# Performance work log

Measured on AMD Instinct MI355X. Metric: run time of the kernel, lower is better.

## Reference

```python
import jax, jax.numpy as jnp
import numpy as np

HEADS = 16
DIM_HEAD = 64
SCALE = DIM_HEAD ** -0.5
TEMPERATURE = 1.0
CAUSAL = True


def setup_inputs() -> dict:
    key = jax.random.key(0)
    k_x, k_qkv, k_out, k_len = jax.random.split(key, 4)
    B, N, D = 2, 2048, 1024
    inner = HEADS * DIM_HEAD  # 1024
    x = jax.random.normal(k_x, (B, N, D), dtype=jnp.float32)
    # realistic key-padding mask: True for valid tokens (variable lengths)
    lengths = jax.random.randint(k_len, (B,), N // 2, N + 1)
    mask = jnp.arange(N)[None, :] < lengths[:, None]  # (B, N) bool
    W_qkv = jax.random.normal(k_qkv, (D, 3 * inner), dtype=jnp.float32) * (D ** -0.5)
    W_out = jax.random.normal(k_out, (inner, D), dtype=jnp.float32) * (inner ** -0.5)
    b_out = jnp.zeros((D,), dtype=jnp.float32)
    return {"x": x, "mask": mask, "W_qkv": W_qkv, "W_out": W_out, "b_out": b_out}


def reference(x, mask, W_qkv, W_out, b_out):
    B, N, D = x.shape
    qkv = x @ W_qkv  # (B, N, 3*inner)
    q, k, v = jnp.split(qkv, 3, axis=-1)
    # (B, N, H*d) -> (B, H, N, d)
    def split_heads(t):
        return t.reshape(B, N, HEADS, DIM_HEAD).transpose(0, 2, 1, 3)
    q, k, v = split_heads(q), split_heads(k), split_heads(v)
    q = q * SCALE
    dots = jnp.einsum('bhid,bhjd->bhij', q, k)  # (B, H, N, N)
    mask_value = -jnp.finfo(dots.dtype).max
    # key padding mask: True = valid; mask invalid keys
    dots = jnp.where(mask[:, None, None, :], dots, mask_value)
    if CAUSAL:
        causal = jnp.arange(N)[None, :] > jnp.arange(N)[:, None]  # True = future -> masked
        dots = jnp.where(causal[None, None, :, :], mask_value, dots)
    # stable softmax with temperature (jax.nn.softmax subtracts max internally)
    attn = jax.nn.softmax(dots / TEMPERATURE, axis=-1)
    out = jnp.einsum('bhij,bhjd->bhid', attn, v)  # (B, H, N, d)
    out = out.transpose(0, 2, 1, 3).reshape(B, N, HEADS * DIM_HEAD)
    return out @ W_out + b_out
```

## Files before the change

kernel.cpp:

```cpp
#include <hip/hip_runtime.h>

#define BATCH   2
#define NSEQ    2048
#define DMODEL  1024
#define HEADS   16
#define DHEAD   64
#define INNER   1024
#define NCOL    3072
#define BNROWS  4096
#define KDIM    1024

typedef unsigned short ushort;
typedef unsigned int   uint;
typedef __attribute__((ext_vector_type(8)))  short  short8;
typedef __attribute__((ext_vector_type(4)))  float  f32x4;
typedef __attribute__((ext_vector_type(16))) float  f32x16;
typedef __attribute__((ext_vector_type(8)))  ushort ushort8;
typedef __attribute__((ext_vector_type(4)))  float  f4v;
typedef __attribute__((ext_vector_type(4)))  uint   uint4v;

#define QSCALE 0.1803368801111204f

__device__ __forceinline__ ushort f2bf(float f) {
  uint u = __builtin_bit_cast(uint, f);
  u += 0x7fffu + ((u >> 16) & 1u);
  return (ushort)(u >> 16);
}
__device__ __forceinline__ uint cvtpk(float a, float b) {
  uint r;
  asm("v_cvt_pk_bf16_f32 %0, %1, %2" : "=v"(r) : "v"(a), "v"(b));
  return r;
}

__device__ __forceinline__ f32x4 mfma16(short8 a, short8 b, f32x4 c) {
  return __builtin_amdgcn_mfma_f32_16x16x32_bf16(a, b, c, 0, 0, 0);
}
__device__ __forceinline__ f32x16 mfma32(short8 a, short8 b, f32x16 c) {
  return __builtin_amdgcn_mfma_f32_32x32x16_bf16(a, b, c, 0, 0, 0);
}

#define GLDS(gp, lp) __builtin_amdgcn_global_load_lds( \
    (const __attribute__((address_space(1))) void*)(gp), \
    (__attribute__((address_space(3))) void*)(lp), 16, 0, 0)

__global__ __launch_bounds__(256) void lens_kernel(const int* __restrict__ mask,
                                                   int* __restrict__ lens) {
  __shared__ int sm[256];
  int b = blockIdx.x, t = threadIdx.x;
  int s = 0;
  for (int i = t; i < NSEQ; i += 256) s += (mask[b * NSEQ + i] != 0);
  sm[t] = s;
  __syncthreads();
  for (int off = 128; off > 0; off >>= 1) {
    if (t < off) sm[t] += sm[t + off];
    __syncthreads();
  }
  if (t == 0) lens[b] = sm[0];
}

__global__ __launch_bounds__(256) void cast_bf16_kernel(const float* __restrict__ x,
                                                        ushort* __restrict__ y, int n8) {
  int i = blockIdx.x * 256 + threadIdx.x;
  if (i >= n8) return;
  const f4v* xv = (const f4v*)x;
  f4v a = xv[(size_t)i * 2], b = xv[(size_t)i * 2 + 1];
  ushort8 o;
  o[0] = f2bf(a[0]); o[1] = f2bf(a[1]); o[2] = f2bf(a[2]); o[3] = f2bf(a[3]);
  o[4] = f2bf(b[0]); o[5] = f2bf(b[1]); o[6] = f2bf(b[2]); o[7] = f2bf(b[3]);
  ((ushort8*)y)[i] = o;
}

__global__ __launch_bounds__(256) void transpose_bf16_kernel(const float* __restrict__ W,
                                                             ushort* __restrict__ Wt,
                                                             int K, int C) {
  __shared__ float tile[32][33];
  int c0 = blockIdx.x * 32, k0 = blockIdx.y * 32;
  int tx = threadIdx.x, ty = threadIdx.y;
#pragma unroll
  for (int i = 0; i < 4; ++i)
    tile[ty + i * 8][tx] = W[(size_t)(k0 + ty + i * 8) * C + c0 + tx];
  __syncthreads();
#pragma unroll
  for (int i = 0; i < 4; ++i)
    Wt[(size_t)(c0 + ty + i * 8) * K + k0 + tx] = f2bf(tile[tx][ty + i * 8]);
}

__global__ __launch_bounds__(256) void vtrans_kernel(const ushort* __restrict__ v,
                                                     ushort* __restrict__ vt) {
  __shared__ ushort t[32][34];
  int d0 = blockIdx.x * 32, n0 = blockIdx.y * 32, bh = blockIdx.z;
  const ushort* vb  = v  + (size_t)bh * NSEQ * DHEAD;
  ushort*       vtb = vt + (size_t)bh * NSEQ * DHEAD;
  int tx = threadIdx.x, ty = threadIdx.y;
#pragma unroll
  for (int i = 0; i < 4; ++i)
    t[ty + i * 8][tx] = vb[(size_t)(n0 + ty + i * 8) * DHEAD + d0 + tx];
  __syncthreads();
#pragma unroll
  for (int i = 0; i < 4; ++i)
    vtb[(size_t)(d0 + ty + i * 8) * NSEQ + n0 + tx] = t[tx][ty + i * 8];
}

template <int EPI>
__global__ __launch_bounds__(256) void gemm_bt_kernel(
    const ushort* __restrict__ A, const ushort* __restrict__ Bt,
    ushort* __restrict__ q_out, ushort* __restrict__ k_out, ushort* __restrict__ v_out,
    const float* __restrict__ bias, float* __restrict__ outp) {
  __shared__ __align__(16) ushort lA[128 * 64];
  __shared__ __align__(16) ushort lB[128 * 64];
  const int tid = threadIdx.x;
  const int wv = tid >> 6, lane = tid & 63;
  const int wr = wv >> 1, wc = wv & 1;
  const int m0 = blockIdx.x * 128, n0 = blockIdx.y * 128;
  const int l15 = lane & 15, l4 = lane >> 4;

  f32x4 zero = {0.f, 0.f, 0.f, 0.f};
  f32x4 acc[4][4];
#pragma unroll
  for (int i = 0; i < 4; ++i)
#pragma unroll
    for (int j = 0; j < 4; ++j) acc[i][j] = zero;

  const char* Ab  = (const char*)A;
  const char* Bb  = (const char*)Bt;
  char* lAb = (char*)lA;
  char* lBb = (char*)lB;

  for (int kt = 0; kt < KDIM; kt += 64) {
#pragma unroll
    for (int t = 0; t < 4; ++t) {
      int o = wv * 4096 + t * 1024 + lane * 16;
      int row = o >> 7, cb = o & 127;
      GLDS(Ab + ((size_t)(m0 + row) * KDIM + kt) * 2 + cb, lAb + o);
      GLDS(Bb + ((size_t)(n0 + row) * KDIM + kt) * 2 + cb, lBb + o);
    }
    __syncthreads();

    short8 af[4][2], bfr[4][2];
#pragma unroll
    for (int i = 0; i < 4; ++i) {
#pragma unroll
      for (int kc = 0; kc < 2; ++kc) {
        af[i][kc]  = *(const short8*)(lAb + (wr * 64 + i * 16 + l15) * 128 + kc * 64 + l4 * 16);
        bfr[i][kc] = *(const short8*)(lBb + (wc * 64 + i * 16 + l15) * 128 + kc * 64 + l4 * 16);
      }
    }
#pragma unroll
    for (int i = 0; i < 4; ++i)
#pragma unroll
      for (int j = 0; j < 4; ++j)
#pragma unroll
        for (int kc = 0; kc < 2; ++kc)
          acc[i][j] = mfma16(af[i][kc], bfr[j][kc], acc[i][j]);
    __syncthreads();
  }

#pragma unroll
  for (int i = 0; i < 4; ++i) {
#pragma unroll
    for (int j = 0; j < 4; ++j) {
#pragma unroll
      for (int r = 0; r < 4; ++r) {
        int grow = m0 + wr * 64 + i * 16 + l4 * 4 + r;
        int gcol = n0 + wc * 64 + j * 16 + l15;
        float v = acc[i][j][r];
        if (EPI == 0) {
          int b = grow >> 11, n = grow & (NSEQ - 1);
          int which = gcol >> 10, inner = gcol & 1023;
          int h = inner >> 6, dd = inner & 63;
          size_t off = ((size_t)(b * HEADS + h) * NSEQ + n) * DHEAD + dd;
          if (which == 0)
            q_out[off] = f2bf(v * QSCALE);
          else if (which == 1)
            k_out[off] = f2bf(v);
          else
            v_out[off] = f2bf(v);
        } else {
          outp[(size_t)grow * INNER + gcol] = v + bias[gcol];
        }
      }
    }
  }
}

__global__ __launch_bounds__(64) void attn_kernel(
    const ushort* __restrict__ q, const ushort* __restrict__ k,
    const ushort* __restrict__ vt, const int* __restrict__ lens,
    ushort* __restrict__ ctx) {
  const int lane = threadIdx.x;
  const int l31 = lane & 31, hi = lane >> 5;
  const int bid = blockIdx.x;
  const int bh = bid & 31, qt = bid >> 5;
  const int b = bh >> 4, h = bh & 15;
  const int len = lens[b];
  const ushort* qb  = q  + (size_t)bh * NSEQ * DHEAD;
  const ushort* kbp = k  + (size_t)bh * NSEQ * DHEAD;
  const ushort* vtb = vt + (size_t)bh * DHEAD * NSEQ;

  const int qglob = qt * 32 + l31;
  const int qcap  = min(qglob, len - 1);

  short8 qf[4];
#pragma unroll
  for (int dk = 0; dk < 4; ++dk)
    qf[dk] = *(const short8*)&qb[(size_t)(qt * 32 + l31) * DHEAD + dk * 16 + hi * 8];

  f32x16 Ot[2];
#pragma unroll
  for (int d0b = 0; d0b < 2; ++d0b)
#pragma unroll
    for (int r = 0; r < 16; ++r) Ot[d0b][r] = 0.f;
  float mrow = -3.0e38f, lsum = 0.f;

  const int kbend = min(qt, (len - 1) >> 5);

  short8 kf[4], kn[4];
#pragma unroll
  for (int dk = 0; dk < 4; ++dk)
    kf[dk] = *(const short8*)&kbp[(size_t)l31 * DHEAD + dk * 16 + hi * 8];

  for (int kb = 0; kb <= kbend; ++kb) {
    f32x16 S;
#pragma unroll
    for (int r = 0; r < 16; ++r) S[r] = 0.f;
#pragma unroll
    for (int dk = 0; dk < 4; ++dk) S = mfma32(kf[dk], qf[dk], S);

    short8 vf[2][2];
#pragma unroll
    for (int d0b = 0; d0b < 2; ++d0b)
#pragma unroll
      for (int ks = 0; ks < 2; ++ks)
        vf[d0b][ks] = *(const short8*)&vtb[(size_t)(d0b * 32 + l31) * NSEQ +
                                           kb * 32 + ks * 16 + hi * 8];

    {
      int kread = min(kb + 1, kbend);
#pragma unroll
      for (int dk = 0; dk < 4; ++dk)
        kn[dk] = *(const short8*)&kbp[(size_t)(kread * 32 + l31) * DHEAD + dk * 16 + hi * 8];
    }

    bool fast = (kb < qt) && (kb * 32 + 31 < len);
    if (!fast) {
      int base = kb * 32 + 4 * hi;
#pragma unroll
      for (int r = 0; r < 16; ++r) {
        int c = (r & 3) + 8 * (r >> 2);
        if (base + c > qcap) S[r] = -3.0e38f;
      }
    }

    float t0 = fmaxf(S[0], S[1]),  t1 = fmaxf(S[2], S[3]);
    float t2 = fmaxf(S[4], S[5]),  t3 = fmaxf(S[6], S[7]);
    float t4 = fmaxf(S[8], S[9]),  t5 = fmaxf(S[10], S[11]);
    float t6 = fmaxf(S[12], S[13]), t7 = fmaxf(S[14], S[15]);
    t0 = fmaxf(t0, t1); t2 = fmaxf(t2, t3); t4 = fmaxf(t4, t5); t6 = fmaxf(t6, t7);
    float pm = fmaxf(fmaxf(t0, t2), fmaxf(t4, t6));
    pm = fmaxf(pm, __shfl_xor(pm, 32));

    if (!__all(pm <= mrow + 8.0f)) {
      float mnew = fmaxf(mrow, pm);
      float scale = exp2f(mrow - mnew);
      lsum *= scale;
#pragma unroll
      for (int d0b = 0; d0b < 2; ++d0b)
#pragma unroll
        for (int r = 0; r < 16; ++r) Ot[d0b][r] *= scale;
      mrow = mnew;
    }

    float p[16];
#pragma unroll
    for (int r = 0; r < 16; ++r) p[r] = exp2f(S[r] - mrow);
    float s0 = (p[0] + p[1]) + (p[2] + p[3]);
    float s1 = (p[4] + p[5]) + (p[6] + p[7]);
    float s2 = (p[8] + p[9]) + (p[10] + p[11]);
    float s3 = (p[12] + p[13]) + (p[14] + p[15]);
    float rs = (s0 + s1) + (s2 + s3);
    rs += __shfl_xor(rs, 32);
    lsum += rs;

    uint Pw[8], Xw[8];
#pragma unroll
    for (int i = 0; i < 8; ++i) Pw[i] = cvtpk(p[2 * i], p[2 * i + 1]);
#pragma unroll
    for (int i = 0; i < 8; ++i) Xw[i] = __shfl_xor(Pw[i], 32);
    uint4v bw0 = { hi ? Xw[2] : Pw[0], hi ? Xw[3] : Pw[1],
                   hi ? Pw[2] : Xw[0], hi ? Pw[3] : Xw[1] };
    uint4v bw1 = { hi ? Xw[6] : Pw[4], hi ? Xw[7] : Pw[5],
                   hi ? Pw[6] : Xw[4], hi ? Pw[7] : Xw[5] };
    short8 pb0 = __builtin_bit_cast(short8, bw0);
    short8 pb1 = __builtin_bit_cast(short8, bw1);

#pragma unroll
    for (int d0b = 0; d0b < 2; ++d0b) {
      Ot[d0b] = mfma32(vf[d0b][0], pb0, Ot[d0b]);
      Ot[d0b] = mfma32(vf[d0b][1], pb1, Ot[d0b]);
    }

#pragma unroll
    for (int dk = 0; dk < 4; ++dk) kf[dk] = kn[dk];
  }

  float inv = 1.0f / lsum;
  size_t rowbase = ((size_t)(b * NSEQ) + qglob) * INNER + h * DHEAD;
#pragma unroll
  for (int d0b = 0; d0b < 2; ++d0b) {
#pragma unroll
    for (int i = 0; i < 8; ++i) {
      int d = 2 * (i & 1) + 8 * (i >> 1) + 4 * hi;
      uint w = cvtpk(Ot[d0b][2 * i] * inv, Ot[d0b][2 * i + 1] * inv);
      *(uint*)&ctx[rowbase + d0b * 32 + d] = w;
    }
  }
}

extern "C" void kernel_launch(void* const* d_in, const int* in_sizes, int n_in,
                              void* d_out, int out_size, void* d_ws, size_t ws_size,
                              hipStream_t stream) {
  const float* x    = (const float*)d_in[0];
  const int*   mask = (const int*)d_in[1];
  const float* Wqkv = (const float*)d_in[2];
  const float* Wout = (const float*)d_in[3];
  const float* bias = (const float*)d_in[4];
  float* out = (float*)d_out;

  const size_t QKV_ELEMS = (size_t)BATCH * HEADS * NSEQ * DHEAD;

  ushort* ws = (ushort*)d_ws;
  ushort* x_bf  = ws;
  ushort* wq_t  = x_bf  + (size_t)BNROWS * DMODEL;
  ushort* wo_t  = wq_t  + (size_t)NCOL * KDIM;
  ushort* q_bf  = wo_t  + (size_t)INNER * KDIM;
  ushort* k_bf  = q_bf  + QKV_ELEMS;
  ushort* v_bf  = k_bf  + QKV_ELEMS;
  ushort* ctx   = v_bf  + QKV_ELEMS;
  int* lens = (int*)(ctx + (size_t)BNROWS * INNER);
  ushort* vt_bf = x_bf;

  lens_kernel<<<dim3(BATCH), dim3(256), 0, stream>>>(mask, lens);
  cast_bf16_kernel<<<dim3((BNROWS * DMODEL / 8 + 255) / 256), dim3(256), 0, stream>>>(
      x, x_bf, BNROWS * DMODEL / 8);
  transpose_bf16_kernel<<<dim3(NCOL / 32, KDIM / 32), dim3(32, 8), 0, stream>>>(
      Wqkv, wq_t, KDIM, NCOL);
  transpose_bf16_kernel<<<dim3(INNER / 32, KDIM / 32), dim3(32, 8), 0, stream>>>(
      Wout, wo_t, KDIM, INNER);

  gemm_bt_kernel<0><<<dim3(BNROWS / 128, NCOL / 128), dim3(256), 0, stream>>>(
      x_bf, wq_t, q_bf, k_bf, v_bf, nullptr, nullptr);

  vtrans_kernel<<<dim3(DHEAD / 32, NSEQ / 32, BATCH * HEADS), dim3(32, 8), 0, stream>>>(
      v_bf, vt_bf);

  attn_kernel<<<dim3((NSEQ / 32) * BATCH * HEADS), dim3(64), 0, stream>>>(
      q_bf, k_bf, vt_bf, lens, ctx);

  gemm_bt_kernel<1><<<dim3(BNROWS / 128, INNER / 128), dim3(256), 0, stream>>>(
      ctx, wo_t, nullptr, nullptr, nullptr, bias, out);
}
```

Baseline: 237.5 us.

## Split attention key loop across two waves with LDS softmax merge

Each attention block now runs two waves that process alternating 32-key tiles of the causal range, halving the serial key loop per query tile. At the end, wave 1 writes its partial output accumulators, row max and row sum to shared memory, and wave 0 rescales and merges them flash-decoding style before writing the context. This aims to shorten the critical path of long causal rows and raise the number of active waves. The cost is an LDS round-trip, a block barrier and extra registers per block.

```diff
diff --git a/kernel.cpp b/kernel.cpp
--- a/kernel.cpp
+++ b/kernel.cpp
@@ -183,11 +183,13 @@
   }
 }
 
-__global__ __launch_bounds__(64) void attn_kernel(
+__global__ __launch_bounds__(128, 4) void attn_kernel(
     const ushort* __restrict__ q, const ushort* __restrict__ k,
     const ushort* __restrict__ vt, const int* __restrict__ lens,
     ushort* __restrict__ ctx) {
-  const int lane = threadIdx.x;
+  __shared__ float lred[64 * 33 + 64];
+  const int tid  = threadIdx.x;
+  const int wave = tid >> 6, lane = tid & 63;
   const int l31 = lane & 31, hi = lane >> 5;
   const int bid = blockIdx.x;
   const int bh = bid & 31, qt = bid >> 5;
@@ -215,11 +217,14 @@
   const int kbend = min(qt, (len - 1) >> 5);
 
   short8 kf[4], kn[4];
-#pragma unroll
-  for (int dk = 0; dk < 4; ++dk)
-    kf[dk] = *(const short8*)&kbp[(size_t)l31 * DHEAD + dk * 16 + hi * 8];
-
-  for (int kb = 0; kb <= kbend; ++kb) {
+  {
+    int k0t = min(wave, kbend);
+#pragma unroll
+    for (int dk = 0; dk < 4; ++dk)
+      kf[dk] = *(const short8*)&kbp[(size_t)(k0t * 32 + l31) * DHEAD + dk * 16 + hi * 8];
+  }
+
+  for (int kb = wave; kb <= kbend; kb += 2) {
     f32x16 S;
 #pragma unroll
     for (int r = 0; r < 16; ++r) S[r] = 0.f;
@@ -235,7 +240,7 @@
                                            kb * 32 + ks * 16 + hi * 8];
 
     {
-      int kread = min(kb + 1, kbend);
+      int kread = min(kb + 2, kbend);
 #pragma unroll
       for (int dk = 0; dk < 4; ++dk)
         kn[dk] = *(const short8*)&kbp[(size_t)(kread * 32 + l31) * DHEAD + dk * 16 + hi * 8];
@@ -303,15 +308,35 @@
     for (int dk = 0; dk < 4; ++dk) kf[dk] = kn[dk];
   }
 
-  float inv = 1.0f / lsum;
-  size_t rowbase = ((size_t)(b * NSEQ) + qglob) * INNER + h * DHEAD;
-#pragma unroll
-  for (int d0b = 0; d0b < 2; ++d0b) {
-#pragma unroll
-    for (int i = 0; i < 8; ++i) {
-      int d = 2 * (i & 1) + 8 * (i >> 1) + 4 * hi;
-      uint w = cvtpk(Ot[d0b][2 * i] * inv, Ot[d0b][2 * i + 1] * inv);
-      *(uint*)&ctx[rowbase + d0b * 32 + d] = w;
+  if (wave == 1) {
+#pragma unroll
+    for (int d0b = 0; d0b < 2; ++d0b)
+#pragma unroll
+      for (int r = 0; r < 16; ++r) lred[lane * 33 + d0b * 16 + r] = Ot[d0b][r];
+    if (hi == 0) {
+      lred[64 * 33 + l31]      = mrow;
+      lred[64 * 33 + 32 + l31] = lsum;
+    }
+  }
+  __syncthreads();
+  if (wave == 0) {
+    float m1 = lred[64 * 33 + l31];
+    float l1 = lred[64 * 33 + 32 + l31];
+    float ms = fmaxf(mrow, m1);
+    float al = exp2f(mrow - ms);
+    float be = exp2f(m1 - ms);
+    float lt = lsum * al + l1 * be;
+    float inv = 1.0f / lt;
+    size_t rowbase = ((size_t)(b * NSEQ) + qglob) * INNER + h * DHEAD;
+#pragma unroll
+    for (int d0b = 0; d0b < 2; ++d0b) {
+#pragma unroll
+      for (int i = 0; i < 8; ++i) {
+        float oa = (Ot[d0b][2 * i]     * al + lred[lane * 33 + d0b * 16 + 2 * i]     * be) * inv;
+        float ob = (Ot[d0b][2 * i + 1] * al + lred[lane * 33 + d0b * 16 + 2 * i + 1] * be) * inv;
+        int d = 2 * (i & 1) + 8 * (i >> 1) + 4 * hi;
+        *(uint*)&ctx[rowbase + d0b * 32 + d] = cvtpk(oa, ob);
+      }
     }
   }
 }
@@ -353,7 +378,7 @@
   vtrans_kernel<<<dim3(DHEAD / 32, NSEQ / 32, BATCH * HEADS), dim3(32, 8), 0, stream>>>(
       v_bf, vt_bf);
 
-  attn_kernel<<<dim3((NSEQ / 32) * BATCH * HEADS), dim3(64), 0, stream>>>(
+  attn_kernel<<<dim3((NSEQ / 32) * BATCH * HEADS), dim3(128), 0, stream>>>(
       q_bf, k_bf, vt_bf, lens, ctx);
 
   gemm_bt_kernel<1><<<dim3(BNROWS / 128, INNER / 128), dim3(256), 0, stream>>>(
```

After: 237.4 us. About the same (-0.0%).
